# Kernel optimization log

Hardware: AMD Instinct MI355X
Metric: run time of the kernel (lower is better)

## Reference

```python
import jax, jax.numpy as jnp
import numpy as np

D_PAIR = 128
N_HEAD = 4
D_HID = 32
SCALING = 1.0 / np.sqrt(D_HID)


def setup_inputs() -> dict:
    key = jax.random.key(0)
    ks = jax.random.split(key, 12)
    B, L = 1, 256
    s = 0.02
    return {
        "pair": jax.random.normal(ks[0], (B, L, L, D_PAIR), dtype=jnp.float32),
        "gamma": jnp.ones((D_PAIR,), jnp.float32),
        "beta": jnp.zeros((D_PAIR,), jnp.float32),
        "Wq": jax.random.normal(ks[1], (D_PAIR, N_HEAD * D_HID), jnp.float32) * s,
        "Wk": jax.random.normal(ks[2], (D_PAIR, N_HEAD * D_HID), jnp.float32) * s,
        "Wv": jax.random.normal(ks[3], (D_PAIR, N_HEAD * D_HID), jnp.float32) * s,
        "Wb": jax.random.normal(ks[4], (D_PAIR, N_HEAD), jnp.float32) * s,
        "Wg": jax.random.normal(ks[5], (D_PAIR, N_HEAD * D_HID), jnp.float32) * s,
        "bg": jnp.ones((N_HEAD * D_HID,), jnp.float32),
        "Wo": jax.random.normal(ks[6], (N_HEAD * D_HID, D_PAIR), jnp.float32) * s,
        "bo": jnp.zeros((D_PAIR,), jnp.float32),
    }


def _layernorm(x, gamma, beta, eps=1e-5):
    mu = jnp.mean(x, axis=-1, keepdims=True)
    var = jnp.var(x, axis=-1, keepdims=True)
    return (x - mu) * jax.lax.rsqrt(var + eps) * gamma + beta


def reference(pair, gamma, beta, Wq, Wk, Wv, Wb, Wg, bg, Wo, bo):
    B, L = pair.shape[:2]
    x = _layernorm(pair, gamma, beta)                      # (B,L,L,D)
    q = (x @ Wq).reshape(B, L, L, N_HEAD, D_HID) * SCALING  # (B,L,L,h,d)
    k = (x @ Wk).reshape(B, L, L, N_HEAD, D_HID)
    v = (x @ Wv).reshape(B, L, L, N_HEAD, D_HID)
    bias = x @ Wb                                           # (B,L,L,h)
    gate = jax.nn.sigmoid(x @ Wg + bg)                      # (B,L,L,h*d)
    # start_node=True: attend over ending index k of row i
    attn = jnp.einsum('bijhd,bikhd->bijkh', q, k)           # (B,L,L,L,h)
    attn = attn + bias[:, None]                             # bias[b,j,k,h] broadcast over i
    attn = jax.nn.softmax(attn, axis=-2)                    # over k
    out = jnp.einsum('bijkh,bikhd->bijhd', attn, v).reshape(B, L, L, N_HEAD * D_HID)
    out = gate * out
    return out @ Wo + bo
```

## Files before the change

### kernel.cpp

```cpp
#include <hip/hip_runtime.h>
#include <math.h>

#define L 256
#define DP 128
#define NH 4
#define DH 32
#define NROW 65536

typedef unsigned short ushort_t;
typedef __attribute__((ext_vector_type(8))) short short8;
typedef __attribute__((ext_vector_type(4))) float f32x4;

constexpr float SCALING = 0.17677669529663687f;

static __device__ __forceinline__ unsigned short f2bf(float f) {
    unsigned u = __builtin_bit_cast(unsigned, f);
    u = u + 0x7fffu + ((u >> 16) & 1u);
    return (unsigned short)(u >> 16);
}
static __device__ __forceinline__ float bf2f(unsigned short h) {
    unsigned u = ((unsigned)h) << 16;
    return __builtin_bit_cast(float, u);
}

__global__ __launch_bounds__(256) void prep_kernel(
    const float* __restrict__ Wq, const float* __restrict__ Wk, const float* __restrict__ Wv,
    const float* __restrict__ Wb, const float* __restrict__ Wg, const float* __restrict__ Wo,
    ushort_t* __restrict__ WtAll, ushort_t* __restrict__ WohT, ushort_t* __restrict__ WolT)
{
    int rowi = blockIdx.x * 16 + (threadIdx.x >> 4);
    int d0 = (threadIdx.x & 15) * 8;
    #pragma unroll
    for (int dd = 0; dd < 8; ++dd) {
        int d = d0 + dd;
        if (rowi < 512) {
            int n = rowi & 127;
            float val;
            if (rowi < 128)      val = Wq[d * 128 + n] * SCALING;
            else if (rowi < 256) val = Wk[d * 128 + n];
            else if (rowi < 384) val = Wv[d * 128 + n];
            else                 val = Wg[d * 128 + n];
            WtAll[rowi * 128 + d] = f2bf(val);
        } else if (rowi < 516) {
            WtAll[rowi * 128 + d] = f2bf(Wb[d * 4 + (rowi - 512)]);
        } else if (rowi < 528) {
            WtAll[rowi * 128 + d] = 0;
        } else if (rowi < 656) {
            int n = rowi - 528;
            WohT[n * 128 + d] = f2bf(Wo[d * 128 + n]);
        } else {
            int n = rowi - 656;
            float wv = Wo[d * 128 + n];
            unsigned short hb = f2bf(wv);
            WolT[n * 128 + d] = f2bf(wv - bf2f(hb));
        }
    }
}

__global__ __launch_bounds__(256) void ln_proj_mfma(
    const float* __restrict__ pair, const float* __restrict__ gamma, const float* __restrict__ beta,
    const ushort_t* __restrict__ WtAll, const float* __restrict__ bgv,
    ushort_t* __restrict__ qo, ushort_t* __restrict__ ko, ushort_t* __restrict__ vo,
    float* __restrict__ gateo, float* __restrict__ biasT)
{
    __shared__ __align__(16) unsigned char xs[64 * 256];

    const int t = threadIdx.x;
    const int w = t >> 6, lane = t & 63;
    const int c = lane & 15, g = lane >> 4;
    const int base = blockIdx.x * 64;

    {
        const float* pr = pair + ((size_t)base + w * 16) * DP;
        float e0[16], e1[16];
        #pragma unroll
        for (int r = 0; r < 16; ++r) {
            e0[r] = pr[r * DP + lane];
            e1[r] = pr[r * DP + 64 + lane];
        }
        const float g0 = gamma[lane], g1 = gamma[lane + 64];
        const float b0 = beta[lane],  b1 = beta[lane + 64];
        #pragma unroll
        for (int r = 0; r < 16; ++r) {
            float s = e0[r] + e1[r], ss = e0[r] * e0[r] + e1[r] * e1[r];
            #pragma unroll
            for (int o = 32; o > 0; o >>= 1) { s += __shfl_xor(s, o); ss += __shfl_xor(ss, o); }
            float mu = s * (1.f / DP);
            float rq = rsqrtf(ss * (1.f / DP) - mu * mu + 1e-5f);
            int rl = w * 16 + r;
            unsigned swz = (unsigned)((rl & 7) << 4);
            *(ushort_t*)(xs + (((unsigned)(rl * 256 + 2 * lane)) ^ swz)) = f2bf((e0[r] - mu) * rq * g0 + b0);
            *(ushort_t*)(xs + (((unsigned)(rl * 256 + 2 * (lane + 64))) ^ swz)) = f2bf((e1[r] - mu) * rq * g1 + b1);
        }
    }
    __syncthreads();

    const int mtot = (w == 3) ? 9 : 8;
    for (int m = 0; m < mtot; ++m) {
        const int nt = (m < 8) ? (w + 4 * m) : 32;
        const ushort_t* wbp = WtAll + (size_t)(nt * 16 + c) * 128 + 8 * g;
        short8 bw[4];
        #pragma unroll
        for (int kk = 0; kk < 4; ++kk) bw[kk] = *(const short8*)(wbp + kk * 32);

        const int n = nt * 16 + c;
        #pragma unroll
        for (int rg = 0; rg < 4; ++rg) {
            const int rl = rg * 16 + c;
            const unsigned swz = (unsigned)((rl & 7) << 4);
            f32x4 acc = {0.f, 0.f, 0.f, 0.f};
            #pragma unroll
            for (int kk = 0; kk < 4; ++kk) {
                short8 af = *(const short8*)(xs + (((unsigned)(rl * 256 + kk * 64 + g * 16)) ^ swz));
                acc = __builtin_amdgcn_mfma_f32_16x16x32_bf16(af, bw[kk], acc, 0, 0, 0);
            }
            const int rowb = base + rg * 16 + 4 * g;
            if (nt < 8) {
                #pragma unroll
                for (int e = 0; e < 4; ++e) qo[(size_t)(rowb + e) * 128 + n] = f2bf(acc[e]);
            } else if (nt < 16) {
                #pragma unroll
                for (int e = 0; e < 4; ++e) ko[(size_t)(rowb + e) * 128 + (n - 128)] = f2bf(acc[e]);
            } else if (nt < 24) {
                #pragma unroll
                for (int e = 0; e < 4; ++e) vo[(size_t)(rowb + e) * 128 + (n - 256)] = f2bf(acc[e]);
            } else if (nt < 32) {
                float bgn = bgv[n - 384];
                #pragma unroll
                for (int e = 0; e < 4; ++e)
                    gateo[(size_t)(rowb + e) * 128 + (n - 384)] = 1.f / (1.f + __expf(-(acc[e] + bgn)));
            } else {
                if (c < 4) {
                    #pragma unroll
                    for (int e = 0; e < 4; ++e) {
                        int r = rowb + e;
                        biasT[(size_t)c * NROW + (r & 255) * 256 + (r >> 8)] = acc[e];
                    }
                }
            }
        }
    }
}

__global__ __launch_bounds__(256) void attn_mfma(
    const ushort_t* __restrict__ qbf, const ushort_t* __restrict__ kbf, const ushort_t* __restrict__ vbf,
    const float* __restrict__ biasT, float* __restrict__ ao)
{
    __shared__ __align__(16) unsigned char Kb[256 * 64];
    __shared__ __align__(16) unsigned char Vt[32 * 512];
    __shared__ __align__(16) unsigned char Plds[4 * 64 * 80];

    const int h = blockIdx.x & 3, i = blockIdx.x >> 2;
    const int t = threadIdx.x, w = t >> 6, lane = t & 63;
    const int c = lane & 15, g = lane >> 4;

    {
        const ushort_t* kg = kbf + (size_t)(i * 256) * 128 + h * 32;
        #pragma unroll
        for (int it = 0; it < 8; ++it) {
            int idx = it * 256 + t;
            int kr = idx >> 3, dp = idx & 7;
            *(uint2*)(Kb + kr * 64 + dp * 8) = *(const uint2*)(kg + (size_t)kr * 128 + dp * 4);
        }
    }
    {
        const ushort_t* vg = vbf + (size_t)(i * 256) * 128 + h * 32;
        #pragma unroll
        for (int it = 0; it < 4; ++it) {
            int idx = it * 256 + t;
            int kp = idx >> 3, dp = idx & 7;
            int kt = kp >> 4, cc = kp & 15;
            int r0 = kt * 32 + cc;
            uint2 a = *(const uint2*)(vg + (size_t)r0 * 128 + dp * 4);
            uint2 b = *(const uint2*)(vg + (size_t)(r0 + 16) * 128 + dp * 4);
            unsigned av[4] = { a.x & 0xffffu, a.x >> 16, a.y & 0xffffu, a.y >> 16 };
            unsigned bv[4] = { b.x & 0xffffu, b.x >> 16, b.y & 0xffffu, b.y >> 16 };
            int kcolb = kt * 64 + 4 * cc;
            #pragma unroll
            for (int dd = 0; dd < 4; ++dd) {
                int d = 4 * dp + dd;
                unsigned pk = (bv[dd] << 16) | av[dd];
                *(unsigned*)(Vt + (((unsigned)(d * 512 + kcolb)) ^ ((unsigned)((d & 7) << 4)))) = pk;
            }
        }
    }
    __syncthreads();

    const int j0 = w * 64;
    short8 qf[4];
    {
        const ushort_t* qg = qbf + (size_t)(i * 256 + j0) * 128 + h * 32;
        #pragma unroll
        for (int jt = 0; jt < 4; ++jt)
            qf[jt] = *(const short8*)(qg + (size_t)(jt * 16 + c) * 128 + 8 * g);
    }

    unsigned char* Pw = Plds + w * 5120;
    const float* biasTh = biasT + (size_t)h * NROW;

    f32x4 O[4][2];
    f32x4 rsum[4];
    #pragma unroll
    for (int jt = 0; jt < 4; ++jt) {
        rsum[jt] = (f32x4){0.f, 0.f, 0.f, 0.f};
        O[jt][0] = (f32x4){0.f, 0.f, 0.f, 0.f};
        O[jt][1] = (f32x4){0.f, 0.f, 0.f, 0.f};
    }

    for (int kt = 0; kt < 8; ++kt) {
        short8 kf[2];
        #pragma unroll
        for (int ks = 0; ks < 2; ++ks)
            kf[ks] = *(const short8*)(Kb + (kt * 32 + ks * 16 + c) * 64 + g * 16);

        f32x4 s[4][2];
        #pragma unroll
        for (int jt = 0; jt < 4; ++jt) {
            #pragma unroll
            for (int ks = 0; ks < 2; ++ks) {
                f32x4 z = {0.f, 0.f, 0.f, 0.f};
                s[jt][ks] = __builtin_amdgcn_mfma_f32_16x16x32_bf16(qf[jt], kf[ks], z, 0, 0, 0);
            }
        }
        #pragma unroll
        for (int jt = 0; jt < 4; ++jt) {
            #pragma unroll
            for (int ks = 0; ks < 2; ++ks) {
                const f32x4 bv = *(const f32x4*)(biasTh + (size_t)(kt * 32 + ks * 16 + c) * 256 + (j0 + jt * 16 + 4 * g));
                #pragma unroll
                for (int e = 0; e < 4; ++e)
                    s[jt][ks][e] = __expf(s[jt][ks][e] + bv[e]);
            }
            #pragma unroll
            for (int e = 0; e < 4; ++e) {
                rsum[jt][e] += s[jt][0][e] + s[jt][1][e];
                unsigned pk = ((unsigned)f2bf(s[jt][1][e]) << 16) | (unsigned)f2bf(s[jt][0][e]);
                *(unsigned*)(Pw + (jt * 16 + 4 * g + e) * 80 + 4 * c) = pk;
            }
        }
        short8 vb0, vb1;
        {
            int d_0 = c, d_1 = 16 + c;
            vb0 = *(const short8*)(Vt + (((unsigned)(d_0 * 512 + kt * 64 + g * 16)) ^ ((unsigned)((d_0 & 7) << 4))));
            vb1 = *(const short8*)(Vt + (((unsigned)(d_1 * 512 + kt * 64 + g * 16)) ^ ((unsigned)((d_1 & 7) << 4))));
        }
        #pragma unroll
        for (int jt = 0; jt < 4; ++jt) {
            short8 pa = *(const short8*)(Pw + (jt * 16 + c) * 80 + g * 16);
            O[jt][0] = __builtin_amdgcn_mfma_f32_16x16x32_bf16(pa, vb0, O[jt][0], 0, 0, 0);
            O[jt][1] = __builtin_amdgcn_mfma_f32_16x16x32_bf16(pa, vb1, O[jt][1], 0, 0, 0);
        }
    }

    #pragma unroll
    for (int jt = 0; jt < 4; ++jt) {
        #pragma unroll
        for (int e = 0; e < 4; ++e) {
            float v = rsum[jt][e];
            v += __shfl_xor(v, 1); v += __shfl_xor(v, 2);
            v += __shfl_xor(v, 4); v += __shfl_xor(v, 8);
            rsum[jt][e] = 1.f / v;
        }
    }
    float* aoB = ao + (size_t)(i * 256 + j0) * 128 + h * 32;
    #pragma unroll
    for (int jt = 0; jt < 4; ++jt) {
        #pragma unroll
        for (int dt = 0; dt < 2; ++dt) {
            #pragma unroll
            for (int e = 0; e < 4; ++e)
                aoB[(size_t)(jt * 16 + 4 * g + e) * 128 + dt * 16 + c] = O[jt][dt][e] * rsum[jt][e];
        }
    }
}

__global__ __launch_bounds__(256) void out_proj_mfma(
    const float* __restrict__ gate, const float* __restrict__ ao,
    const ushort_t* __restrict__ WohT, const ushort_t* __restrict__ WolT,
    const float* __restrict__ bo, float* __restrict__ out)
{
    const int t = threadIdx.x;
    const int w = t >> 6, lane = t & 63;
    const int c = lane & 15, g = lane >> 4;
    const int base = blockIdx.x * 64;

    const size_t arow = (size_t)(base + w * 16 + c) * 128;
    short8 ah[4], al[4];
    #pragma unroll
    for (int kk = 0; kk < 4; ++kk) {
        const float* gp = gate + arow + kk * 32 + g * 8;
        const float* ap = ao + arow + kk * 32 + g * 8;
        f32x4 g0 = *(const f32x4*)gp, g1 = *(const f32x4*)(gp + 4);
        f32x4 a0 = *(const f32x4*)ap, a1 = *(const f32x4*)(ap + 4);
        short8 hv, lv;
        #pragma unroll
        for (int e = 0; e < 4; ++e) {
            float x0 = g0[e] * a0[e];
            float x1 = g1[e] * a1[e];
            unsigned short h0 = f2bf(x0), h1 = f2bf(x1);
            hv[e] = (short)h0; hv[e + 4] = (short)h1;
            lv[e] = (short)f2bf(x0 - bf2f(h0)); lv[e + 4] = (short)f2bf(x1 - bf2f(h1));
        }
        ah[kk] = hv; al[kk] = lv;
    }

    const int rowb = base + w * 16 + 4 * g;
    #pragma unroll 2
    for (int nt = 0; nt < 8; ++nt) {
        f32x4 acc = {0.f, 0.f, 0.f, 0.f};
        const ushort_t* wh = WohT + (size_t)(nt * 16 + c) * 128 + 8 * g;
        const ushort_t* wl = WolT + (size_t)(nt * 16 + c) * 128 + 8 * g;
        #pragma unroll
        for (int kk = 0; kk < 4; ++kk) {
            short8 bh = *(const short8*)(wh + kk * 32);
            short8 bl = *(const short8*)(wl + kk * 32);
            acc = __builtin_amdgcn_mfma_f32_16x16x32_bf16(ah[kk], bh, acc, 0, 0, 0);
            acc = __builtin_amdgcn_mfma_f32_16x16x32_bf16(ah[kk], bl, acc, 0, 0, 0);
            acc = __builtin_amdgcn_mfma_f32_16x16x32_bf16(al[kk], bh, acc, 0, 0, 0);
        }
        int n = nt * 16 + c;
        float bon = bo[n];
        #pragma unroll
        for (int e = 0; e < 4; ++e)
            out[(size_t)(rowb + e) * 128 + n] = acc[e] + bon;
    }
}

extern "C" void kernel_launch(void* const* d_in, const int* in_sizes, int n_in,
                              void* d_out, int out_size, void* d_ws, size_t ws_size,
                              hipStream_t stream) {
    const float* pair  = (const float*)d_in[0];
    const float* gamma = (const float*)d_in[1];
    const float* beta  = (const float*)d_in[2];
    const float* Wq    = (const float*)d_in[3];
    const float* Wk    = (const float*)d_in[4];
    const float* Wv    = (const float*)d_in[5];
    const float* Wb    = (const float*)d_in[6];
    const float* Wg    = (const float*)d_in[7];
    const float* bg    = (const float*)d_in[8];
    const float* Wo    = (const float*)d_in[9];
    const float* bo    = (const float*)d_in[10];

    unsigned char* ws = (unsigned char*)d_ws;
    size_t off = 0;
    ushort_t* q_bf   = (ushort_t*)(ws + off); off += (size_t)NROW * 128 * 2;
    ushort_t* k_bf   = (ushort_t*)(ws + off); off += (size_t)NROW * 128 * 2;
    ushort_t* v_bf   = (ushort_t*)(ws + off); off += (size_t)NROW * 128 * 2;
    float*    gateo  = (float*)(ws + off);    off += (size_t)NROW * 128 * 4;
    float*    ao     = (float*)(ws + off);    off += (size_t)NROW * 128 * 4;
    float*    biasT  = (float*)(ws + off);    off += (size_t)NH * NROW * 4;
    ushort_t* WtAll  = (ushort_t*)(ws + off); off += 528 * 128 * 2;
    ushort_t* WohT   = (ushort_t*)(ws + off); off += 128 * 128 * 2;
    ushort_t* WolT   = (ushort_t*)(ws + off); off += 128 * 128 * 2;

    prep_kernel<<<49, 256, 0, stream>>>(Wq, Wk, Wv, Wb, Wg, Wo, WtAll, WohT, WolT);
    ln_proj_mfma<<<NROW / 64, 256, 0, stream>>>(pair, gamma, beta, WtAll, bg,
                                                q_bf, k_bf, v_bf, gateo, biasT);
    attn_mfma<<<L * NH, 256, 0, stream>>>(q_bf, k_bf, v_bf, biasT, ao);
    out_proj_mfma<<<NROW / 64, 256, 0, stream>>>(gateo, ao, WohT, WolT, bo, (float*)d_out);
}
```

Measured before the change: 239.5 us.

## Compute transposed attention scores to keep P in registers, skipping LDS round-trip

Swaps MFMA operand order so scores come out as S^T. Each lane then holds the k-values its P operand needs, so the P tile is packed into bf16 registers and fed straight into the PV MFMA with no shared-memory write and read. To match, bias is stored untransposed (row j, contiguous k) and loaded as vectors, and V rows are permuted when staged to LDS to fit the new k ordering. Output is computed transposed, allowing vectorized f32x4 stores and a shorter row-sum reduction. The risk is correctness of the k-index permutation in the V staging.

```diff
diff --git a/kernel.cpp b/kernel.cpp
--- a/kernel.cpp
+++ b/kernel.cpp
@@ -10,6 +10,7 @@
 typedef unsigned short ushort_t;
 typedef __attribute__((ext_vector_type(8))) short short8;
 typedef __attribute__((ext_vector_type(4))) float f32x4;
+typedef __attribute__((ext_vector_type(4))) unsigned int u32x4;
 
 constexpr float SCALING = 0.17677669529663687f;
 
@@ -21,6 +22,9 @@
 static __device__ __forceinline__ float bf2f(unsigned short h) {
     unsigned u = ((unsigned)h) << 16;
     return __builtin_bit_cast(float, u);
+}
+static __device__ __forceinline__ unsigned packbf(float lo, float hi) {
+    return ((unsigned)f2bf(hi) << 16) | (unsigned)f2bf(lo);
 }
 
 __global__ __launch_bounds__(256) void prep_kernel(
@@ -132,10 +136,8 @@
             } else {
                 if (c < 4) {
                     #pragma unroll
-                    for (int e = 0; e < 4; ++e) {
-                        int r = rowb + e;
-                        biasT[(size_t)c * NROW + (r & 255) * 256 + (r >> 8)] = acc[e];
-                    }
+                    for (int e = 0; e < 4; ++e)
+                        biasT[(size_t)c * NROW + rowb + e] = acc[e];
                 }
             }
         }
@@ -148,7 +150,6 @@
 {
     __shared__ __align__(16) unsigned char Kb[256 * 64];
     __shared__ __align__(16) unsigned char Vt[32 * 512];
-    __shared__ __align__(16) unsigned char Plds[4 * 64 * 80];
 
     const int h = blockIdx.x & 3, i = blockIdx.x >> 2;
     const int t = threadIdx.x, w = t >> 6, lane = t & 63;
@@ -170,11 +171,13 @@
             int idx = it * 256 + t;
             int kp = idx >> 3, dp = idx & 7;
             int kt = kp >> 4, cc = kp & 15;
-            int r0 = kt * 32 + cc;
-            uint2 a = *(const uint2*)(vg + (size_t)r0 * 128 + dp * 4);
-            uint2 b = *(const uint2*)(vg + (size_t)(r0 + 16) * 128 + dp * 4);
-            unsigned av[4] = { a.x & 0xffffu, a.x >> 16, a.y & 0xffffu, a.y >> 16 };
-            unsigned bv[4] = { b.x & 0xffffu, b.x >> 16, b.y & 0xffffu, b.y >> 16 };
+            int a = cc & 3, gg = cc >> 2;
+            int k1 = (a < 2) ? (4 * gg + 2 * a) : (12 + 4 * gg + 2 * a);
+            int r0 = kt * 32 + k1;
+            uint2 va = *(const uint2*)(vg + (size_t)r0 * 128 + dp * 4);
+            uint2 vb = *(const uint2*)(vg + (size_t)(r0 + 1) * 128 + dp * 4);
+            unsigned av[4] = { va.x & 0xffffu, va.x >> 16, va.y & 0xffffu, va.y >> 16 };
+            unsigned bv[4] = { vb.x & 0xffffu, vb.x >> 16, vb.y & 0xffffu, vb.y >> 16 };
             int kcolb = kt * 64 + 4 * cc;
             #pragma unroll
             for (int dd = 0; dd < 4; ++dd) {
@@ -195,14 +198,12 @@
             qf[jt] = *(const short8*)(qg + (size_t)(jt * 16 + c) * 128 + 8 * g);
     }
 
-    unsigned char* Pw = Plds + w * 5120;
-    const float* biasTh = biasT + (size_t)h * NROW;
+    const float* biasH = biasT + (size_t)h * NROW;
 
     f32x4 O[4][2];
-    f32x4 rsum[4];
+    float rsum[4] = {0.f, 0.f, 0.f, 0.f};
     #pragma unroll
     for (int jt = 0; jt < 4; ++jt) {
-        rsum[jt] = (f32x4){0.f, 0.f, 0.f, 0.f};
         O[jt][0] = (f32x4){0.f, 0.f, 0.f, 0.f};
         O[jt][1] = (f32x4){0.f, 0.f, 0.f, 0.f};
     }
@@ -212,64 +213,54 @@
         #pragma unroll
         for (int ks = 0; ks < 2; ++ks)
             kf[ks] = *(const short8*)(Kb + (kt * 32 + ks * 16 + c) * 64 + g * 16);
-
-        f32x4 s[4][2];
+        short8 vb0 = *(const short8*)(Vt + (((unsigned)(c * 512 + kt * 64 + g * 16)) ^ ((unsigned)((c & 7) << 4))));
+        short8 vb1 = *(const short8*)(Vt + (((unsigned)((16 + c) * 512 + kt * 64 + g * 16)) ^ ((unsigned)(((16 + c) & 7) << 4))));
+
         #pragma unroll
         for (int jt = 0; jt < 4; ++jt) {
-            #pragma unroll
-            for (int ks = 0; ks < 2; ++ks) {
+            f32x4 s0, s1;
+            {
                 f32x4 z = {0.f, 0.f, 0.f, 0.f};
-                s[jt][ks] = __builtin_amdgcn_mfma_f32_16x16x32_bf16(qf[jt], kf[ks], z, 0, 0, 0);
-            }
-        }
-        #pragma unroll
-        for (int jt = 0; jt < 4; ++jt) {
-            #pragma unroll
-            for (int ks = 0; ks < 2; ++ks) {
-                const f32x4 bv = *(const f32x4*)(biasTh + (size_t)(kt * 32 + ks * 16 + c) * 256 + (j0 + jt * 16 + 4 * g));
-                #pragma unroll
-                for (int e = 0; e < 4; ++e)
-                    s[jt][ks][e] = __expf(s[jt][ks][e] + bv[e]);
-            }
+                s0 = __builtin_amdgcn_mfma_f32_16x16x32_bf16(kf[0], qf[jt], z, 0, 0, 0);
+                s1 = __builtin_amdgcn_mfma_f32_16x16x32_bf16(kf[1], qf[jt], z, 0, 0, 0);
+            }
+            const int jrow = j0 + jt * 16 + c;
+            const f32x4 b0 = *(const f32x4*)(biasH + (size_t)jrow * 256 + kt * 32 + 4 * g);
+            const f32x4 b1 = *(const f32x4*)(biasH + (size_t)jrow * 256 + kt * 32 + 16 + 4 * g);
             #pragma unroll
             for (int e = 0; e < 4; ++e) {
-                rsum[jt][e] += s[jt][0][e] + s[jt][1][e];
-                unsigned pk = ((unsigned)f2bf(s[jt][1][e]) << 16) | (unsigned)f2bf(s[jt][0][e]);
-                *(unsigned*)(Pw + (jt * 16 + 4 * g + e) * 80 + 4 * c) = pk;
-            }
-        }
-        short8 vb0, vb1;
-        {
-            int d_0 = c, d_1 = 16 + c;
-            vb0 = *(const short8*)(Vt + (((unsigned)(d_0 * 512 + kt * 64 + g * 16)) ^ ((unsigned)((d_0 & 7) << 4))));
-            vb1 = *(const short8*)(Vt + (((unsigned)(d_1 * 512 + kt * 64 + g * 16)) ^ ((unsigned)((d_1 & 7) << 4))));
-        }
-        #pragma unroll
-        for (int jt = 0; jt < 4; ++jt) {
-            short8 pa = *(const short8*)(Pw + (jt * 16 + c) * 80 + g * 16);
-            O[jt][0] = __builtin_amdgcn_mfma_f32_16x16x32_bf16(pa, vb0, O[jt][0], 0, 0, 0);
-            O[jt][1] = __builtin_amdgcn_mfma_f32_16x16x32_bf16(pa, vb1, O[jt][1], 0, 0, 0);
+                s0[e] = __expf(s0[e] + b0[e]);
+                s1[e] = __expf(s1[e] + b1[e]);
+            }
+            rsum[jt] += (s0[0] + s0[1] + s0[2] + s0[3]) + (s1[0] + s1[1] + s1[2] + s1[3]);
+            u32x4 pk;
+            pk[0] = packbf(s0[0], s0[1]);
+            pk[1] = packbf(s0[2], s0[3]);
+            pk[2] = packbf(s1[0], s1[1]);
+            pk[3] = packbf(s1[2], s1[3]);
+            short8 pa = __builtin_bit_cast(short8, pk);
+            O[jt][0] = __builtin_amdgcn_mfma_f32_16x16x32_bf16(vb0, pa, O[jt][0], 0, 0, 0);
+            O[jt][1] = __builtin_amdgcn_mfma_f32_16x16x32_bf16(vb1, pa, O[jt][1], 0, 0, 0);
         }
     }
 
     #pragma unroll
     for (int jt = 0; jt < 4; ++jt) {
-        #pragma unroll
-        for (int e = 0; e < 4; ++e) {
-            float v = rsum[jt][e];
-            v += __shfl_xor(v, 1); v += __shfl_xor(v, 2);
-            v += __shfl_xor(v, 4); v += __shfl_xor(v, 8);
-            rsum[jt][e] = 1.f / v;
-        }
+        float v = rsum[jt];
+        v += __shfl_xor(v, 16);
+        v += __shfl_xor(v, 32);
+        rsum[jt] = 1.f / v;
     }
     float* aoB = ao + (size_t)(i * 256 + j0) * 128 + h * 32;
     #pragma unroll
     for (int jt = 0; jt < 4; ++jt) {
+        const float inv = rsum[jt];
         #pragma unroll
         for (int dt = 0; dt < 2; ++dt) {
-            #pragma unroll
-            for (int e = 0; e < 4; ++e)
-                aoB[(size_t)(jt * 16 + 4 * g + e) * 128 + dt * 16 + c] = O[jt][dt][e] * rsum[jt][e];
+            f32x4 ov;
+            #pragma unroll
+            for (int e = 0; e < 4; ++e) ov[e] = O[jt][dt][e] * inv;
+            *(f32x4*)(aoB + (size_t)(jt * 16 + c) * 128 + dt * 16 + 4 * g) = ov;
         }
     }
 }
```

Measured after the change: 232.4 us. 1.03x faster.
